# Performance work log

Measured on AMD Instinct MI355X. Metric: run time of the kernel, lower is better.

The kernel has to match this reference:

```python
import jax, jax.numpy as jnp
import numpy as np

N, E, G = 20000, 320000, 8
H, C = 4, 64
NODE_IN, EDGE_IN, HID = 18, 4, 64
NEG = 0.2    # GATv2 leaky_relu negative slope
EPS = 1e-5   # BatchNorm eps (eval mode: running_mean=0, running_var=1)


def setup_inputs() -> dict:
    key = jax.random.key(0)
    ks = iter(jax.random.split(key, 48))
    rn = lambda shape, s=0.05: jax.random.normal(next(ks), shape, dtype=jnp.float32) * s
    return {
        "x": jax.random.normal(next(ks), (N, NODE_IN), dtype=jnp.float32),
        "edge_attr": jax.random.uniform(next(ks), (E, EDGE_IN), dtype=jnp.float32),
        "enc_w1": rn((NODE_IN, HID)), "enc_b1": jnp.zeros((HID,), jnp.float32),
        "enc_w2": rn((HID, HID)), "enc_b2": jnp.zeros((HID,), jnp.float32),
        "g1_wl": rn((HID, H * C)), "g1_wr": rn((HID, H * C)), "g1_we": rn((EDGE_IN, H * C)),
        "g1_att": rn((H, C)), "g1_b": jnp.zeros((H * C,), jnp.float32),
        "bn1_g": jnp.ones((H * C,), jnp.float32), "bn1_b": jnp.zeros((H * C,), jnp.float32),
        "g2_wl": rn((H * C, H * C)), "g2_wr": rn((H * C, H * C)), "g2_we": rn((EDGE_IN, H * C)),
        "g2_att": rn((H, C)), "g2_b": jnp.zeros((C,), jnp.float32),
        "bn2_g": jnp.ones((C,), jnp.float32), "bn2_b": jnp.zeros((C,), jnp.float32),
        "sage_wl": rn((HID, HID)), "sage_bl": jnp.zeros((HID,), jnp.float32), "sage_wr": rn((HID, HID)),
        "bn3_g": jnp.ones((HID,), jnp.float32), "bn3_b": jnp.zeros((HID,), jnp.float32),
        "gh_w1": rn((2 * HID, HID)), "gh_b1": jnp.zeros((HID,), jnp.float32),
        "gh_w2": rn((HID, 32)), "gh_b2": jnp.zeros((32,), jnp.float32),
        "gh_w3": rn((32, 1)), "gh_b3": jnp.zeros((1,), jnp.float32),
        "eh_w1": rn((2 * HID + EDGE_IN, 32)), "eh_b1": jnp.zeros((32,), jnp.float32),
        "eh_w2": rn((32, 1)), "eh_b2": jnp.zeros((1,), jnp.float32),
        "edge_index": jax.random.randint(next(ks), (2, E), 0, N, dtype=jnp.int32),
        "batch": jnp.sort(jax.random.randint(next(ks), (N,), 0, G, dtype=jnp.int32)),
    }


def _segment_softmax(logits, seg, num):
    mx = jax.ops.segment_max(logits, seg, num_segments=num)
    ex = jnp.exp(logits - mx[seg])
    den = jax.ops.segment_sum(ex, seg, num_segments=num)
    return ex / den[seg]


def _gatv2(h, src, dst, ea, wl, wr, we, att, bias, concat):
    n = h.shape[0]
    xl = (h @ wl).reshape(n, H, C)   # messages come from x_l[src]
    xr = (h @ wr).reshape(n, H, C)
    ee = (ea @ we).reshape(-1, H, C)
    m = xl[src] + xr[dst] + ee                                    # [E', H, C]
    logit = jnp.einsum('ehc,hc->eh', jax.nn.leaky_relu(m, NEG), att)
    alpha = _segment_softmax(logit, dst, n)                       # [E', H]
    out = jax.ops.segment_sum(alpha[:, :, None] * xl[src], dst, num_segments=n)
    if concat:
        return out.reshape(n, H * C) + bias
    return out.mean(axis=1) + bias


def _bn_eval(h, g, b):
    # eval-mode BatchNorm with running_mean=0, running_var=1
    return h * (g / jnp.sqrt(1.0 + EPS)) + b


def reference(x, edge_attr, enc_w1, enc_b1, enc_w2, enc_b2,
              g1_wl, g1_wr, g1_we, g1_att, g1_b, bn1_g, bn1_b,
              g2_wl, g2_wr, g2_we, g2_att, g2_b, bn2_g, bn2_b,
              sage_wl, sage_bl, sage_wr, bn3_g, bn3_b,
              gh_w1, gh_b1, gh_w2, gh_b2, gh_w3, gh_b3,
              eh_w1, eh_b1, eh_w2, eh_b2, edge_index, batch):
    src, dst = edge_index[0], edge_index[1]
    # PyG add_self_loops with fill_value='mean': loop edge_attr = mean of incoming edge_attr
    ones = jnp.ones((E,), jnp.float32)
    cnt = jax.ops.segment_sum(ones, dst, num_segments=N)
    loop_attr = jax.ops.segment_sum(edge_attr, dst, num_segments=N) / jnp.clip(cnt, 1.0)[:, None]
    sl = jnp.arange(N, dtype=src.dtype)
    src_sl = jnp.concatenate([src, sl])
    dst_sl = jnp.concatenate([dst, sl])
    ea_sl = jnp.concatenate([edge_attr, loop_attr], axis=0)

    # ZoneEncoder (dropout inactive in eval)
    h = jax.nn.relu(x @ enc_w1 + enc_b1) @ enc_w2 + enc_b2
    h = _gatv2(h, src_sl, dst_sl, ea_sl, g1_wl, g1_wr, g1_we, g1_att, g1_b, True)
    h = jax.nn.elu(_bn_eval(h, bn1_g, bn1_b))
    h = _gatv2(h, src_sl, dst_sl, ea_sl, g2_wl, g2_wr, g2_we, g2_att, g2_b, False)
    h = jax.nn.elu(_bn_eval(h, bn2_g, bn2_b))
    # SAGEConv: lin_l(mean_{j->i} h_j) + lin_r(h_i), no self loops
    agg = jax.ops.segment_sum(h[src], dst, num_segments=N) / jnp.clip(cnt, 1.0)[:, None]
    h = agg @ sage_wl + sage_bl + h @ sage_wr
    h = jax.nn.relu(_bn_eval(h, bn3_g, bn3_b))
    # global mean + max pooling per graph
    cntg = jax.ops.segment_sum(jnp.ones((N,), jnp.float32), batch, num_segments=G)
    mean_p = jax.ops.segment_sum(h, batch, num_segments=G) / jnp.clip(cntg, 1.0)[:, None]
    max_p = jax.ops.segment_max(h, batch, num_segments=G)
    hp = jnp.concatenate([mean_p, max_p], axis=-1)                # [G, 128]
    z = jax.nn.relu(hp @ gh_w1 + gh_b1)
    z = jax.nn.relu(z @ gh_w2 + gh_b2)
    graph_score = jax.nn.sigmoid(z @ gh_w3 + gh_b3)               # [G, 1]
    ef = jnp.concatenate([h[src], h[dst], edge_attr], axis=-1)    # [E, 132]
    ez = jax.nn.relu(ef @ eh_w1 + eh_b1)
    edge_scores = jax.nn.sigmoid(ez @ eh_w2 + eh_b2)              # [E, 1]
    return (graph_score, edge_scores)
```

## Files before the change

kernel.cpp:

```cpp
#include <hip/hip_runtime.h>

#define NN 20000
#define NE 320000
#define EP (NE + NN)
#define NG 8
#define HC 256
#define NODE_IN 18
#define HID 64
#define NEG_SLOPE 0.2f
#define BN_EPS 1e-5f

#define OFF_XL    0u
#define OFF_XR    5120000u
#define OFF_H1    10240000u
#define OFF_WTL   12800000u
#define OFF_WTR   12832768u
#define OFF_H0    15360000u
#define OFF_H3    16640000u
#define OFF_ZERO  18000000u
#define OFF_CNT   18000000u
#define OFF_PSUM  18020000u
#define OFF_PMAX  18020512u
#define OFF_PCNT  18021024u
#define ZERO_FLOATS (18021040u - 18000000u)
#define OFF_EACSR 18021040u
#define OFF_RP    19381040u
#define OFF_SRC   19421041u
#define OFF_BSUM  19761056u

#define SCAN_ELEM 1024
#define SCAN_NB ((NN + SCAN_ELEM - 1) / SCAN_ELEM)

typedef __attribute__((ext_vector_type(8))) short bf16x8_t;
typedef __attribute__((ext_vector_type(4))) float f32x4_t;

__device__ __forceinline__ ushort f2bf(float f) {
  unsigned u = __float_as_uint(f);
  unsigned r = (u + 0x7fffu + ((u >> 16) & 1u)) >> 16;
  return (ushort)r;
}
__device__ __forceinline__ float bf2f(ushort b) {
  return __uint_as_float(((unsigned)b) << 16);
}

__global__ __launch_bounds__(256) void k_count(
    const int* __restrict__ ei, unsigned* __restrict__ cnt, int* __restrict__ rank) {
  int e = blockIdx.x * 256 + threadIdx.x;
  if (e >= NE) return;
  int d = ei[NE + e];
  rank[e] = (int)atomicAdd(&cnt[d], 1u);
}

__global__ __launch_bounds__(256) void k_cast_wt(
    const float* __restrict__ Wl, const float* __restrict__ Wr,
    ushort* __restrict__ WtL, ushort* __restrict__ WtR) {
  int b = blockIdx.x;
  const float* W = (b < 256) ? Wl : Wr;
  ushort* Wt = (b < 256) ? WtL : WtR;
  int k = b & 255;
  int n = threadIdx.x;
  Wt[n * 256 + k] = f2bf(W[k * 256 + n]);
}

#define ENC_NPW 4
__global__ __launch_bounds__(256) void k_encoder(
    const float* __restrict__ x, const float* __restrict__ w1, const float* __restrict__ b1,
    const float* __restrict__ w2, const float* __restrict__ b2, float* __restrict__ h0) {
  __shared__ float W1[NODE_IN * HID];
  __shared__ float W2[HID * HID];
  __shared__ float B1s[HID];
  __shared__ float B2s[HID];
  __shared__ float hid_s[4][HID];
  const int tid = threadIdx.x;
  for (int i = tid; i < NODE_IN * HID; i += 256) W1[i] = w1[i];
  for (int i = tid; i < HID * HID; i += 256) W2[i] = w2[i];
  if (tid < HID) { B1s[tid] = b1[tid]; B2s[tid] = b2[tid]; }
  __syncthreads();
  const int lane = tid & 63;
  const int w = tid >> 6;
  #pragma unroll
  for (int t = 0; t < ENC_NPW; t++) {
    const int n = blockIdx.x * (4 * ENC_NPW) + w * ENC_NPW + t;
    const float* xp = &x[(size_t)n * NODE_IN];
    float s = B1s[lane];
    #pragma unroll
    for (int i = 0; i < NODE_IN; i++) s += xp[i] * W1[i * HID + lane];
    hid_s[w][lane] = fmaxf(s, 0.f);
    float o = B2s[lane];
    #pragma unroll 8
    for (int k = 0; k < HID; k++) o += hid_s[w][k] * W2[k * HID + lane];
    h0[(size_t)n * HID + lane] = o;
  }
}

__global__ __launch_bounds__(256) void k_scan_blk(
    const unsigned* __restrict__ cnt, int* __restrict__ row_ptr, int* __restrict__ bsums) {
  __shared__ int wsum[4];
  const int tid = threadIdx.x, lane = tid & 63, w = tid >> 6;
  const int i0 = blockIdx.x * SCAN_ELEM + tid * 4;
  int v0 = (i0 + 0 < NN) ? ((int)cnt[i0 + 0] + 1) : 0;
  int v1 = (i0 + 1 < NN) ? ((int)cnt[i0 + 1] + 1) : 0;
  int v2 = (i0 + 2 < NN) ? ((int)cnt[i0 + 2] + 1) : 0;
  int v3 = (i0 + 3 < NN) ? ((int)cnt[i0 + 3] + 1) : 0;
  int tsum = v0 + v1 + v2 + v3;
  int incl = tsum;
  #pragma unroll
  for (int off = 1; off < 64; off <<= 1) {
    int t = __shfl_up(incl, off);
    if (lane >= off) incl += t;
  }
  if (lane == 63) wsum[w] = incl;
  __syncthreads();
  int p = incl - tsum;
  #pragma unroll
  for (int k = 0; k < 4; k++) if (k < w) p += wsum[k];
  if (i0 + 0 < NN) row_ptr[i0 + 0] = p;
  if (i0 + 1 < NN) row_ptr[i0 + 1] = p + v0;
  if (i0 + 2 < NN) row_ptr[i0 + 2] = p + v0 + v1;
  if (i0 + 3 < NN) row_ptr[i0 + 3] = p + v0 + v1 + v2;
  if (tid == 0) bsums[blockIdx.x] = wsum[0] + wsum[1] + wsum[2] + wsum[3];
}

__global__ __launch_bounds__(256) void k_scan_add(
    const int* __restrict__ bsums, int* __restrict__ row_ptr) {
  const int b = blockIdx.x, tid = threadIdx.x;
  int off = 0;
  for (int j = 0; j < b; j++) off += bsums[j];
  const int i0 = b * SCAN_ELEM + tid * 4;
  #pragma unroll
  for (int k = 0; k < 4; k++) {
    int i = i0 + k;
    if (i < NN) row_ptr[i] += off;
  }
  if (b == 0 && tid == 0) row_ptr[NN] = EP;
}

__global__ __launch_bounds__(256) void k_csr_scatter(
    const int* __restrict__ ei, const int* __restrict__ rank,
    const int* __restrict__ row_ptr, const float* __restrict__ ea,
    int* __restrict__ srcs, float* __restrict__ ea_csr) {
  int e = blockIdx.x * 256 + threadIdx.x;
  if (e >= NE) return;
  int s = ei[e], d = ei[NE + e];
  int p = row_ptr[d] + rank[e];
  srcs[p] = s;
  *(float4*)&ea_csr[(size_t)p * 4] = *(const float4*)&ea[(size_t)e * 4];
}

__global__ __launch_bounds__(256) void k_loop_row(
    const int* __restrict__ row_ptr, int* __restrict__ srcs, float* __restrict__ ea_csr) {
  int i = blockIdx.x * 256 + threadIdx.x;
  if (i >= NN) return;
  int start = row_ptr[i], last = row_ptr[i + 1] - 1;
  float sx = 0.f, sy = 0.f, sz = 0.f, sw = 0.f;
  for (int j = start; j < last; ++j) {
    float4 a = *(const float4*)&ea_csr[(size_t)j * 4];
    sx += a.x; sy += a.y; sz += a.z; sw += a.w;
  }
  float c = (float)(last - start);
  if (c < 1.f) c = 1.f;
  float rc = 1.f / c;
  float4 o = {sx * rc, sy * rc, sz * rc, sw * rc};
  *(float4*)&ea_csr[(size_t)last * 4] = o;
  srcs[last] = i | (int)0x80000000;
}

template <int K, int OBF>
__global__ __launch_bounds__(256) void k_gemm256(
    const float* __restrict__ A, const float* __restrict__ W, void* __restrict__ OUTv) {
  __shared__ float Wl[32 * 256];
  __shared__ float Al[32 * 36];
  const int tid = threadIdx.x;
  const int n0 = blockIdx.x * 32;
  const int tx = tid & 63, ty = tid >> 6;
  float acc[8][4];
  #pragma unroll
  for (int m = 0; m < 8; m++)
    #pragma unroll
    for (int c = 0; c < 4; c++) acc[m][c] = 0.f;

  for (int kt = 0; kt < K; kt += 32) {
    #pragma unroll
    for (int r = 0; r < 8; r++) {
      int i4 = tid + 256 * r;
      int row = i4 >> 6;
      int col4 = (i4 & 63) * 4;
      *(float4*)&Wl[row * 256 + col4] = *(const float4*)&W[(size_t)(kt + row) * 256 + col4];
    }
    {
      int m = tid >> 3, kk = (tid & 7) * 4;
      float4 av = *(const float4*)&A[(size_t)(n0 + m) * K + kt + kk];
      Al[(kk + 0) * 36 + m] = av.x;
      Al[(kk + 1) * 36 + m] = av.y;
      Al[(kk + 2) * 36 + m] = av.z;
      Al[(kk + 3) * 36 + m] = av.w;
    }
    __syncthreads();
    #pragma unroll 8
    for (int k = 0; k < 32; k++) {
      float4 b = *(float4*)&Wl[k * 256 + tx * 4];
      float4 a0v = *(float4*)&Al[k * 36 + ty * 8];
      float4 a1v = *(float4*)&Al[k * 36 + ty * 8 + 4];
      float am[8] = {a0v.x, a0v.y, a0v.z, a0v.w, a1v.x, a1v.y, a1v.z, a1v.w};
      #pragma unroll
      for (int m = 0; m < 8; m++) {
        acc[m][0] += am[m] * b.x;
        acc[m][1] += am[m] * b.y;
        acc[m][2] += am[m] * b.z;
        acc[m][3] += am[m] * b.w;
      }
    }
    __syncthreads();
  }
  if (OBF) {
    ushort* OUT = (ushort*)OUTv;
    #pragma unroll
    for (int m = 0; m < 8; m++) {
      ushort4 o = {f2bf(acc[m][0]), f2bf(acc[m][1]), f2bf(acc[m][2]), f2bf(acc[m][3])};
      *(ushort4*)&OUT[(size_t)(n0 + ty * 8 + m) * 256 + tx * 4] = o;
    }
  } else {
    float* OUT = (float*)OUTv;
    #pragma unroll
    for (int m = 0; m < 8; m++) {
      float4 o = {acc[m][0], acc[m][1], acc[m][2], acc[m][3]};
      *(float4*)&OUT[(size_t)(n0 + ty * 8 + m) * 256 + tx * 4] = o;
    }
  }
}

template <int OBF>
__global__ __launch_bounds__(256) void k_gemm_mfma(
    const ushort* __restrict__ A, const ushort* __restrict__ Wt, void* __restrict__ OUTv) {
  __shared__ ushort Asub[32][72];
  __shared__ ushort Wsub[256][72];
  const int tid = threadIdx.x;
  const int lane = tid & 63;
  const int w = tid >> 6;
  const int n0 = blockIdx.x * 32;
  const int lr = lane & 15;
  const int lk = (lane >> 4) * 8;

  f32x4_t acc[2][4];
  #pragma unroll
  for (int m = 0; m < 2; m++)
    #pragma unroll
    for (int n = 0; n < 4; n++) acc[m][n] = (f32x4_t){0.f, 0.f, 0.f, 0.f};

  for (int kt = 0; kt < 256; kt += 64) {
    {
      int r = tid >> 3, seg = (tid & 7) * 8;
      *(uint4*)&Asub[r][seg] = *(const uint4*)&A[(size_t)(n0 + r) * 256 + kt + seg];
    }
    #pragma unroll
    for (int rep = 0; rep < 8; rep++) {
      int idx = rep * 256 + tid;
      int r = idx >> 3, seg = (idx & 7) * 8;
      *(uint4*)&Wsub[r][seg] = *(const uint4*)&Wt[(size_t)r * 256 + kt + seg];
    }
    __syncthreads();
    #pragma unroll
    for (int kk = 0; kk < 2; kk++) {
      bf16x8_t af0 = *(bf16x8_t*)&Asub[lr][kk * 32 + lk];
      bf16x8_t af1 = *(bf16x8_t*)&Asub[16 + lr][kk * 32 + lk];
      #pragma unroll
      for (int n = 0; n < 4; n++) {
        bf16x8_t bfr = *(bf16x8_t*)&Wsub[w * 64 + n * 16 + lr][kk * 32 + lk];
        acc[0][n] = __builtin_amdgcn_mfma_f32_16x16x32_bf16(af0, bfr, acc[0][n], 0, 0, 0);
        acc[1][n] = __builtin_amdgcn_mfma_f32_16x16x32_bf16(af1, bfr, acc[1][n], 0, 0, 0);
      }
    }
    __syncthreads();
  }
  const int crow = (lane >> 4) * 4;
  #pragma unroll
  for (int m = 0; m < 2; m++) {
    #pragma unroll
    for (int n = 0; n < 4; n++) {
      int col = w * 64 + n * 16 + lr;
      #pragma unroll
      for (int r = 0; r < 4; r++) {
        int row = n0 + m * 16 + crow + r;
        if (OBF) ((ushort*)OUTv)[(size_t)row * 256 + col] = f2bf(acc[m][n][r]);
        else     ((float*)OUTv)[(size_t)row * 256 + col] = acc[m][n][r];
      }
    }
  }
}

#define GAT_EDGE(A_, U_, DN_, C0_, C1_, C2_, C3_)                                  \
  {                                                                                \
    float xx_ = bf2f((U_).x), xy_ = bf2f((U_).y), xz_ = bf2f((U_).z), xw_ = bf2f((U_).w); \
    float m0_ = xx_ + xrd.x + (A_).x * we0.x + (A_).y * we1.x + (A_).z * we2.x + (A_).w * we3.x; \
    float m1_ = xy_ + xrd.y + (A_).x * we0.y + (A_).y * we1.y + (A_).z * we2.y + (A_).w * we3.y; \
    float m2_ = xz_ + xrd.z + (A_).x * we0.z + (A_).y * we1.z + (A_).z * we2.z + (A_).w * we3.z; \
    float m3_ = xw_ + xrd.w + (A_).x * we0.w + (A_).y * we1.w + (A_).z * we2.w + (A_).w * we3.w; \
    m0_ = fmaxf(m0_, NEG_SLOPE * m0_);                                             \
    m1_ = fmaxf(m1_, NEG_SLOPE * m1_);                                             \
    m2_ = fmaxf(m2_, NEG_SLOPE * m2_);                                             \
    m3_ = fmaxf(m3_, NEG_SLOPE * m3_);                                             \
    float lg_ = m0_ * attv.x + m1_ * attv.y + m2_ * attv.z + m3_ * attv.w;         \
    lg_ += __shfl_xor(lg_, 1);                                                     \
    lg_ += __shfl_xor(lg_, 2);                                                     \
    lg_ += __shfl_xor(lg_, 4);                                                     \
    lg_ += __shfl_xor(lg_, 8);                                                     \
    float p_ = __expf(lg_);                                                        \
    DN_ += p_;                                                                     \
    C0_ = fmaf(p_, xx_, C0_);                                                      \
    C1_ = fmaf(p_, xy_, C1_);                                                      \
    C2_ = fmaf(p_, xz_, C2_);                                                      \
    C3_ = fmaf(p_, xw_, C3_);                                                      \
  }

template <int CONCAT>
__global__ __launch_bounds__(256) void k_gat_fused(
    const ushort* __restrict__ xl, const float* __restrict__ xr,
    const float* __restrict__ we, const float* __restrict__ att,
    const int* __restrict__ srcs, const float* __restrict__ ea_csr,
    const int* __restrict__ row_ptr,
    const float* __restrict__ bias, const float* __restrict__ bng,
    const float* __restrict__ bnb, void* __restrict__ outp) {
  const int lane = threadIdx.x & 63;
  const int w = threadIdx.x >> 6;
  const int i = blockIdx.x * 4 + w;
  const int c0 = lane * 4;

  const float4 attv = *(const float4*)&att[c0];
  const float4 we0 = *(const float4*)&we[0 * HC + c0];
  const float4 we1 = *(const float4*)&we[1 * HC + c0];
  const float4 we2 = *(const float4*)&we[2 * HC + c0];
  const float4 we3 = *(const float4*)&we[3 * HC + c0];
  const float4 xrd = *(const float4*)&xr[(size_t)i * HC + c0];

  const int start = row_ptr[i];
  const int deg = row_ptr[i + 1] - start;

  float dnA = 0.f, aA0 = 0.f, aA1 = 0.f, aA2 = 0.f, aA3 = 0.f;
  float dnB = 0.f, aB0 = 0.f, aB1 = 0.f, aB2 = 0.f, aB3 = 0.f;

  for (int base = 0; base < deg; base += 64) {
    int rem = deg - base;
    if (rem > 64) rem = 64;
    int sv = 0;
    if (lane < rem) sv = srcs[start + base + lane] & 0x7fffffff;
    int jj = 0;
    for (; jj + 2 <= rem; jj += 2) {
      int s0 = __shfl(sv, jj);
      int s1 = __shfl(sv, jj + 1);
      float4 a0 = *(const float4*)&ea_csr[(size_t)(start + base + jj) * 4];
      float4 a1 = *(const float4*)&ea_csr[(size_t)(start + base + jj + 1) * 4];
      ushort4 u0 = *(const ushort4*)&xl[(size_t)s0 * HC + c0];
      ushort4 u1 = *(const ushort4*)&xl[(size_t)s1 * HC + c0];
      GAT_EDGE(a0, u0, dnA, aA0, aA1, aA2, aA3);
      GAT_EDGE(a1, u1, dnB, aB0, aB1, aB2, aB3);
    }
    if (jj < rem) {
      int s0 = __shfl(sv, jj);
      float4 a0 = *(const float4*)&ea_csr[(size_t)(start + base + jj) * 4];
      ushort4 u0 = *(const ushort4*)&xl[(size_t)s0 * HC + c0];
      GAT_EDGE(a0, u0, dnA, aA0, aA1, aA2, aA3);
    }
  }

  float rinv = 1.f / (dnA + dnB);
  float acc0 = (aA0 + aB0) * rinv;
  float acc1 = (aA1 + aB1) * rinv;
  float acc2 = (aA2 + aB2) * rinv;
  float acc3 = (aA3 + aB3) * rinv;

  const float inv_sqrt = rsqrtf(1.f + BN_EPS);
  if (CONCAT) {
    float4 bi = *(const float4*)&bias[c0];
    float4 g = *(const float4*)&bng[c0];
    float4 bb = *(const float4*)&bnb[c0];
    float v0 = (acc0 + bi.x) * (g.x * inv_sqrt) + bb.x;
    float v1 = (acc1 + bi.y) * (g.y * inv_sqrt) + bb.y;
    float v2 = (acc2 + bi.z) * (g.z * inv_sqrt) + bb.z;
    float v3 = (acc3 + bi.w) * (g.w * inv_sqrt) + bb.w;
    v0 = (v0 > 0.f) ? v0 : (__expf(v0) - 1.f);
    v1 = (v1 > 0.f) ? v1 : (__expf(v1) - 1.f);
    v2 = (v2 > 0.f) ? v2 : (__expf(v2) - 1.f);
    v3 = (v3 > 0.f) ? v3 : (__expf(v3) - 1.f);
    ushort* op = (ushort*)outp;
    ushort4 o = {f2bf(v0), f2bf(v1), f2bf(v2), f2bf(v3)};
    *(ushort4*)&op[(size_t)i * HC + c0] = o;
  } else {
    acc0 += __shfl_xor(acc0, 16); acc0 += __shfl_xor(acc0, 32);
    acc1 += __shfl_xor(acc1, 16); acc1 += __shfl_xor(acc1, 32);
    acc2 += __shfl_xor(acc2, 16); acc2 += __shfl_xor(acc2, 32);
    acc3 += __shfl_xor(acc3, 16); acc3 += __shfl_xor(acc3, 32);
    if (lane < 16) {
      int cc = lane * 4;
      float4 bi = *(const float4*)&bias[cc];
      float4 g = *(const float4*)&bng[cc];
      float4 bb = *(const float4*)&bnb[cc];
      float v0 = (0.25f * acc0 + bi.x) * (g.x * inv_sqrt) + bb.x;
      float v1 = (0.25f * acc1 + bi.y) * (g.y * inv_sqrt) + bb.y;
      float v2 = (0.25f * acc2 + bi.z) * (g.z * inv_sqrt) + bb.z;
      float v3 = (0.25f * acc3 + bi.w) * (g.w * inv_sqrt) + bb.w;
      v0 = (v0 > 0.f) ? v0 : (__expf(v0) - 1.f);
      v1 = (v1 > 0.f) ? v1 : (__expf(v1) - 1.f);
      v2 = (v2 > 0.f) ? v2 : (__expf(v2) - 1.f);
      v3 = (v3 > 0.f) ? v3 : (__expf(v3) - 1.f);
      float* op = (float*)outp;
      float4 o = {v0, v1, v2, v3};
      *(float4*)&op[(size_t)i * 64 + cc] = o;
    }
  }
}

__global__ __launch_bounds__(256) void k_sage(
    const float* __restrict__ h2, const int* __restrict__ row_ptr,
    const int* __restrict__ srcs, const unsigned* __restrict__ cnt,
    const float* __restrict__ wl, const float* __restrict__ bl,
    const float* __restrict__ wr, const float* __restrict__ bng,
    const float* __restrict__ bnb, float* __restrict__ h3) {
  __shared__ float agg_s[4][64];
  __shared__ float h2_s[4][64];
  int lane = threadIdx.x & 63;
  int w = threadIdx.x >> 6;
  int i = blockIdx.x * 4 + w;
  int start = row_ptr[i];
  int nreal = row_ptr[i + 1] - 1 - start;
  float a0 = 0.f, a1 = 0.f, a2 = 0.f, a3 = 0.f;
  for (int base = 0; base < nreal; base += 64) {
    int rem = nreal - base;
    if (rem > 64) rem = 64;
    int sv = 0;
    if (lane < rem) sv = srcs[start + base + lane];
    int jj = 0;
    for (; jj + 4 <= rem; jj += 4) {
      int s0 = __shfl(sv, jj);
      int s1 = __shfl(sv, jj + 1);
      int s2 = __shfl(sv, jj + 2);
      int s3 = __shfl(sv, jj + 3);
      a0 += h2[(size_t)s0 * 64 + lane];
      a1 += h2[(size_t)s1 * 64 + lane];
      a2 += h2[(size_t)s2 * 64 + lane];
      a3 += h2[(size_t)s3 * 64 + lane];
    }
    for (; jj < rem; ++jj) {
      int s0 = __shfl(sv, jj);
      a0 += h2[(size_t)s0 * 64 + lane];
    }
  }
  float a = (a0 + a1) + (a2 + a3);
  float c = (float)cnt[i];
  if (c < 1.f) c = 1.f;
  agg_s[w][lane] = a / c;
  h2_s[w][lane] = h2[(size_t)i * 64 + lane];
  __syncthreads();
  float s = bl[lane];
  #pragma unroll 4
  for (int k = 0; k < 64; k++)
    s += agg_s[w][k] * wl[k * 64 + lane] + h2_s[w][k] * wr[k * 64 + lane];
  s = s * (bng[lane] * rsqrtf(1.f + BN_EPS)) + bnb[lane];
  s = fmaxf(s, 0.f);
  h3[(size_t)i * 64 + lane] = s;
}

__global__ __launch_bounds__(256) void k_pool(
    const float* __restrict__ h3, const int* __restrict__ batch,
    float* __restrict__ psum, float* __restrict__ pmax, float* __restrict__ pcnt) {
  int j = threadIdx.x & 63, grp = threadIdx.x >> 6;
  int nbase = blockIdx.x * 256 + grp * 64;
  float s = 0.f, m = 0.f, cn = 0.f;
  int cur = -1;
  for (int t = 0; t < 64; t++) {
    int n = nbase + t;
    if (n >= NN) break;
    int g = batch[n];
    if (g != cur) {
      if (cur >= 0) {
        atomicAdd(&psum[cur * 64 + j], s);
        atomicMax((int*)&pmax[cur * 64 + j], __float_as_int(m));
        if (j == 0) atomicAdd(&pcnt[cur], cn);
      }
      cur = g; s = 0.f; m = 0.f; cn = 0.f;
    }
    float v = h3[(size_t)n * 64 + j];
    s += v; m = fmaxf(m, v); cn += 1.f;
  }
  if (cur >= 0) {
    atomicAdd(&psum[cur * 64 + j], s);
    atomicMax((int*)&pmax[cur * 64 + j], __float_as_int(m));
    if (j == 0) atomicAdd(&pcnt[cur], cn);
  }
}

__global__ void k_graph_head(
    const float* __restrict__ psum, const float* __restrict__ pmax,
    const float* __restrict__ pcnt,
    const float* __restrict__ w1, const float* __restrict__ b1,
    const float* __restrict__ w2, const float* __restrict__ b2,
    const float* __restrict__ w3, const float* __restrict__ b3,
    float* __restrict__ out) {
  __shared__ float hp[128];
  __shared__ float z1[64];
  __shared__ float z2[32];
  int g = blockIdx.x, j = threadIdx.x;
  float c = pcnt[g];
  if (c < 1.f) c = 1.f;
  hp[j] = psum[g * 64 + j] / c;
  hp[64 + j] = pmax[g * 64 + j];
  __syncthreads();
  float s = b1[j];
  #pragma unroll 8
  for (int k = 0; k < 128; k++) s += hp[k] * w1[k * 64 + j];
  z1[j] = fmaxf(s, 0.f);
  __syncthreads();
  if (j < 32) {
    float s2 = b2[j];
    #pragma unroll 8
    for (int k = 0; k < 64; k++) s2 += z1[k] * w2[k * 32 + j];
    z2[j] = fmaxf(s2, 0.f);
  }
  __syncthreads();
  if (j == 0) {
    float s3 = b3[0];
    #pragma unroll
    for (int k = 0; k < 32; k++) s3 += z2[k] * w3[k];
    out[g] = 1.f / (1.f + expf(-s3));
  }
}

__global__ __launch_bounds__(256) void k_edge_head(
    const float* __restrict__ h3, const int* __restrict__ ei,
    const float* __restrict__ ea,
    const float* __restrict__ w1, const float* __restrict__ b1,
    const float* __restrict__ w2, const float* __restrict__ b2,
    float* __restrict__ out) {
  int e = blockIdx.x * 256 + threadIdx.x;
  if (e >= NE) return;
  int s = ei[e], d = ei[NE + e];
  float acc[32];
  #pragma unroll
  for (int j = 0; j < 32; j++) acc[j] = b1[j];
  const float4* hs = (const float4*)&h3[(size_t)s * 64];
  const float4* hd = (const float4*)&h3[(size_t)d * 64];
  for (int k4 = 0; k4 < 16; k4++) {
    float4 v = hs[k4];
    const float* w = &w1[k4 * 4 * 32];
    #pragma unroll
    for (int j = 0; j < 32; j++) acc[j] += v.x * w[j];
    #pragma unroll
    for (int j = 0; j < 32; j++) acc[j] += v.y * w[32 + j];
    #pragma unroll
    for (int j = 0; j < 32; j++) acc[j] += v.z * w[64 + j];
    #pragma unroll
    for (int j = 0; j < 32; j++) acc[j] += v.w * w[96 + j];
  }
  for (int k4 = 0; k4 < 16; k4++) {
    float4 v = hd[k4];
    const float* w = &w1[(64 + k4 * 4) * 32];
    #pragma unroll
    for (int j = 0; j < 32; j++) acc[j] += v.x * w[j];
    #pragma unroll
    for (int j = 0; j < 32; j++) acc[j] += v.y * w[32 + j];
    #pragma unroll
    for (int j = 0; j < 32; j++) acc[j] += v.z * w[64 + j];
    #pragma unroll
    for (int j = 0; j < 32; j++) acc[j] += v.w * w[96 + j];
  }
  {
    float4 v = *(const float4*)&ea[(size_t)e * 4];
    const float* w = &w1[128 * 32];
    #pragma unroll
    for (int j = 0; j < 32; j++) acc[j] += v.x * w[j];
    #pragma unroll
    for (int j = 0; j < 32; j++) acc[j] += v.y * w[32 + j];
    #pragma unroll
    for (int j = 0; j < 32; j++) acc[j] += v.z * w[64 + j];
    #pragma unroll
    for (int j = 0; j < 32; j++) acc[j] += v.w * w[96 + j];
  }
  float s2 = b2[0];
  #pragma unroll
  for (int j = 0; j < 32; j++) s2 += fmaxf(acc[j], 0.f) * w2[j];
  out[e] = 1.f / (1.f + expf(-s2));
}

extern "C" void kernel_launch(void* const* d_in, const int* in_sizes, int n_in,
                              void* d_out, int out_size, void* d_ws, size_t ws_size,
                              hipStream_t stream) {
  const float* x         = (const float*)d_in[0];
  const float* edge_attr = (const float*)d_in[1];
  const float* enc_w1 = (const float*)d_in[2];
  const float* enc_b1 = (const float*)d_in[3];
  const float* enc_w2 = (const float*)d_in[4];
  const float* enc_b2 = (const float*)d_in[5];
  const float* g1_wl = (const float*)d_in[6];
  const float* g1_wr = (const float*)d_in[7];
  const float* g1_we = (const float*)d_in[8];
  const float* g1_att = (const float*)d_in[9];
  const float* g1_b = (const float*)d_in[10];
  const float* bn1_g = (const float*)d_in[11];
  const float* bn1_b = (const float*)d_in[12];
  const float* g2_wl = (const float*)d_in[13];
  const float* g2_wr = (const float*)d_in[14];
  const float* g2_we = (const float*)d_in[15];
  const float* g2_att = (const float*)d_in[16];
  const float* g2_b = (const float*)d_in[17];
  const float* bn2_g = (const float*)d_in[18];
  const float* bn2_b = (const float*)d_in[19];
  const float* sage_wl = (const float*)d_in[20];
  const float* sage_bl = (const float*)d_in[21];
  const float* sage_wr = (const float*)d_in[22];
  const float* bn3_g = (const float*)d_in[23];
  const float* bn3_b = (const float*)d_in[24];
  const float* gh_w1 = (const float*)d_in[25];
  const float* gh_b1 = (const float*)d_in[26];
  const float* gh_w2 = (const float*)d_in[27];
  const float* gh_b2 = (const float*)d_in[28];
  const float* gh_w3 = (const float*)d_in[29];
  const float* gh_b3 = (const float*)d_in[30];
  const float* eh_w1 = (const float*)d_in[31];
  const float* eh_b1 = (const float*)d_in[32];
  const float* eh_w2 = (const float*)d_in[33];
  const float* eh_b2 = (const float*)d_in[34];
  const int* ei    = (const int*)d_in[35];
  const int* batch = (const int*)d_in[36];
  float* out = (float*)d_out;

  float* ws = (float*)d_ws;
  ushort* xlbf = (ushort*)(ws + OFF_XL);
  float* xr = ws + OFF_XR;
  ushort* h1bf = (ushort*)(ws + OFF_H1);
  ushort* wtl = (ushort*)(ws + OFF_WTL);
  ushort* wtr = (ushort*)(ws + OFF_WTR);
  float* h0 = ws + OFF_H0;
  float* h3 = ws + OFF_H3;
  unsigned* cnt = (unsigned*)(ws + OFF_CNT);
  float* psum = ws + OFF_PSUM;
  float* pmax = ws + OFF_PMAX;
  float* pcnt = ws + OFF_PCNT;
  float* ea_csr = ws + OFF_EACSR;
  int* row_ptr = (int*)(ws + OFF_RP);
  int* srcs = (int*)(ws + OFF_SRC);
  int* bsums = (int*)(ws + OFF_BSUM);
  int* rank = (int*)(ws + OFF_XL);

  hipMemsetAsync(ws + OFF_ZERO, 0, ZERO_FLOATS * sizeof(float), stream);

  k_count<<<NE / 256, 256, 0, stream>>>(ei, cnt, rank);
  k_cast_wt<<<512, 256, 0, stream>>>(g2_wl, g2_wr, wtl, wtr);
  k_encoder<<<NN / (4 * ENC_NPW), 256, 0, stream>>>(x, enc_w1, enc_b1, enc_w2, enc_b2, h0);
  k_scan_blk<<<SCAN_NB, 256, 0, stream>>>(cnt, row_ptr, bsums);
  k_scan_add<<<SCAN_NB, 256, 0, stream>>>(bsums, row_ptr);
  k_csr_scatter<<<NE / 256, 256, 0, stream>>>(ei, rank, row_ptr, edge_attr, srcs, ea_csr);
  k_loop_row<<<(NN + 255) / 256, 256, 0, stream>>>(row_ptr, srcs, ea_csr);

  k_gemm256<64, 1><<<NN / 32, 256, 0, stream>>>(h0, g1_wl, (void*)xlbf);
  k_gemm256<64, 0><<<NN / 32, 256, 0, stream>>>(h0, g1_wr, (void*)xr);
  k_gat_fused<1><<<NN / 4, 256, 0, stream>>>(xlbf, xr, g1_we, g1_att, srcs, ea_csr,
                                             row_ptr, g1_b, bn1_g, bn1_b, (void*)h1bf);

  k_gemm_mfma<1><<<NN / 32, 256, 0, stream>>>(h1bf, wtl, (void*)xlbf);
  k_gemm_mfma<0><<<NN / 32, 256, 0, stream>>>(h1bf, wtr, (void*)xr);
  k_gat_fused<0><<<NN / 4, 256, 0, stream>>>(xlbf, xr, g2_we, g2_att, srcs, ea_csr,
                                             row_ptr, g2_b, bn2_g, bn2_b, (void*)h0);

  k_sage<<<NN / 4, 256, 0, stream>>>(h0, row_ptr, srcs, cnt, sage_wl, sage_bl, sage_wr, bn3_g, bn3_b, h3);

  k_pool<<<(NN + 255) / 256, 256, 0, stream>>>(h3, batch, psum, pmax, pcnt);
  k_graph_head<<<NG, 64, 0, stream>>>(psum, pmax, pcnt, gh_w1, gh_b1, gh_w2, gh_b2, gh_w3, gh_b3, out);
  k_edge_head<<<NE / 256, 256, 0, stream>>>(h3, ei, edge_attr, eh_w1, eh_b1, eh_w2, eh_b2, out + NG);
}
```

Before: 360.3 us.

## Compute edge head MLP with bf16 MFMA on gathered node features

Rewrites the per-edge MLP head so each block gathers 64 edges' source/destination features (from a new bf16 copy of h3 written by the SAGE kernel) plus edge attributes into LDS. It then computes the 132x32 layer with 16x16x32 bf16 MFMA instructions instead of per-thread scalar FMAs over 32 accumulators. A small kernel pre-transposes and zero-pads the head weights to bf16. This removes a heavy scalar-FMA and register-bound workload and halves gather bytes, at the cost of bf16 precision in the edge scores and an extra bf16 store in SAGE.

```diff
diff --git a/kernel.cpp b/kernel.cpp
--- a/kernel.cpp
+++ b/kernel.cpp
@@ -15,6 +15,8 @@
 #define OFF_H1    10240000u
 #define OFF_WTL   12800000u
 #define OFF_WTR   12832768u
+#define OFF_H3B   12865536u
+#define OFF_WT1   13185536u
 #define OFF_H0    15360000u
 #define OFF_H3    16640000u
 #define OFF_ZERO  18000000u
@@ -60,6 +62,13 @@
   int k = b & 255;
   int n = threadIdx.x;
   Wt[n * 256 + k] = f2bf(W[k * 256 + n]);
+}
+
+__global__ __launch_bounds__(256) void k_cast_eh(
+    const float* __restrict__ w1, ushort* __restrict__ wt1) {
+  int idx = blockIdx.x * 256 + threadIdx.x;
+  int n = idx / 192, k = idx - n * 192;
+  wt1[idx] = (k < 132) ? f2bf(w1[k * 32 + n]) : (ushort)0;
 }
 
 #define ENC_NPW 4
@@ -414,7 +423,8 @@
     const int* __restrict__ srcs, const unsigned* __restrict__ cnt,
     const float* __restrict__ wl, const float* __restrict__ bl,
     const float* __restrict__ wr, const float* __restrict__ bng,
-    const float* __restrict__ bnb, float* __restrict__ h3) {
+    const float* __restrict__ bnb, float* __restrict__ h3,
+    ushort* __restrict__ h3b) {
   __shared__ float agg_s[4][64];
   __shared__ float h2_s[4][64];
   int lane = threadIdx.x & 63;
@@ -457,6 +467,7 @@
   s = s * (bng[lane] * rsqrtf(1.f + BN_EPS)) + bnb[lane];
   s = fmaxf(s, 0.f);
   h3[(size_t)i * 64 + lane] = s;
+  h3b[(size_t)i * 64 + lane] = f2bf(s);
 }
 
 __global__ __launch_bounds__(256) void k_pool(
@@ -525,59 +536,71 @@
 }
 
 __global__ __launch_bounds__(256) void k_edge_head(
-    const float* __restrict__ h3, const int* __restrict__ ei,
-    const float* __restrict__ ea,
-    const float* __restrict__ w1, const float* __restrict__ b1,
-    const float* __restrict__ w2, const float* __restrict__ b2,
-    float* __restrict__ out) {
-  int e = blockIdx.x * 256 + threadIdx.x;
-  if (e >= NE) return;
-  int s = ei[e], d = ei[NE + e];
-  float acc[32];
-  #pragma unroll
-  for (int j = 0; j < 32; j++) acc[j] = b1[j];
-  const float4* hs = (const float4*)&h3[(size_t)s * 64];
-  const float4* hd = (const float4*)&h3[(size_t)d * 64];
-  for (int k4 = 0; k4 < 16; k4++) {
-    float4 v = hs[k4];
-    const float* w = &w1[k4 * 4 * 32];
-    #pragma unroll
-    for (int j = 0; j < 32; j++) acc[j] += v.x * w[j];
-    #pragma unroll
-    for (int j = 0; j < 32; j++) acc[j] += v.y * w[32 + j];
-    #pragma unroll
-    for (int j = 0; j < 32; j++) acc[j] += v.z * w[64 + j];
-    #pragma unroll
-    for (int j = 0; j < 32; j++) acc[j] += v.w * w[96 + j];
-  }
-  for (int k4 = 0; k4 < 16; k4++) {
-    float4 v = hd[k4];
-    const float* w = &w1[(64 + k4 * 4) * 32];
-    #pragma unroll
-    for (int j = 0; j < 32; j++) acc[j] += v.x * w[j];
-    #pragma unroll
-    for (int j = 0; j < 32; j++) acc[j] += v.y * w[32 + j];
-    #pragma unroll
-    for (int j = 0; j < 32; j++) acc[j] += v.z * w[64 + j];
-    #pragma unroll
-    for (int j = 0; j < 32; j++) acc[j] += v.w * w[96 + j];
-  }
-  {
-    float4 v = *(const float4*)&ea[(size_t)e * 4];
-    const float* w = &w1[128 * 32];
-    #pragma unroll
-    for (int j = 0; j < 32; j++) acc[j] += v.x * w[j];
-    #pragma unroll
-    for (int j = 0; j < 32; j++) acc[j] += v.y * w[32 + j];
-    #pragma unroll
-    for (int j = 0; j < 32; j++) acc[j] += v.z * w[64 + j];
-    #pragma unroll
-    for (int j = 0; j < 32; j++) acc[j] += v.w * w[96 + j];
-  }
-  float s2 = b2[0];
-  #pragma unroll
-  for (int j = 0; j < 32; j++) s2 += fmaxf(acc[j], 0.f) * w2[j];
-  out[e] = 1.f / (1.f + expf(-s2));
+    const ushort* __restrict__ h3b, const int* __restrict__ ei,
+    const float* __restrict__ ea, const ushort* __restrict__ wt1,
+    const float* __restrict__ b1, const float* __restrict__ w2,
+    const float* __restrict__ b2, float* __restrict__ out) {
+  __shared__ ushort Asub[64][192];
+  __shared__ ushort Wsub[32][192];
+  const int tid = threadIdx.x;
+  const int e0 = blockIdx.x * 64;
+  for (int idx = tid; idx < 768; idx += 256)
+    *(uint4*)&(&Wsub[0][0])[idx * 8] = *(const uint4*)&wt1[idx * 8];
+  for (int idx = tid; idx < 768; idx += 256) {
+    int r = idx / 12, g = idx - r * 12;
+    int e = e0 + r;
+    ushort tmp[16];
+    if (g < 8) {
+      int node = (g < 4) ? ei[e] : ei[NE + e];
+      int gc = (g & 3) * 16;
+      *(uint4*)&tmp[0] = *(const uint4*)&h3b[(size_t)node * 64 + gc];
+      *(uint4*)&tmp[8] = *(const uint4*)&h3b[(size_t)node * 64 + gc + 8];
+    } else if (g == 8) {
+      float4 a = *(const float4*)&ea[(size_t)e * 4];
+      tmp[0] = f2bf(a.x); tmp[1] = f2bf(a.y); tmp[2] = f2bf(a.z); tmp[3] = f2bf(a.w);
+      #pragma unroll
+      for (int j = 4; j < 16; j++) tmp[j] = 0;
+    } else {
+      #pragma unroll
+      for (int j = 0; j < 16; j++) tmp[j] = 0;
+    }
+    *(uint4*)&Asub[r][g * 16] = *(uint4*)&tmp[0];
+    *(uint4*)&Asub[r][g * 16 + 8] = *(uint4*)&tmp[8];
+  }
+  __syncthreads();
+  const int lane = tid & 63, wid = tid >> 6;
+  const int lr = lane & 15, lk = (lane >> 4) * 8;
+  f32x4_t acc0 = (f32x4_t){0.f, 0.f, 0.f, 0.f};
+  f32x4_t acc1 = (f32x4_t){0.f, 0.f, 0.f, 0.f};
+  #pragma unroll
+  for (int ks = 0; ks < 6; ks++) {
+    bf16x8_t af = *(bf16x8_t*)&Asub[wid * 16 + lr][ks * 32 + lk];
+    bf16x8_t bw0 = *(bf16x8_t*)&Wsub[lr][ks * 32 + lk];
+    bf16x8_t bw1 = *(bf16x8_t*)&Wsub[16 + lr][ks * 32 + lk];
+    acc0 = __builtin_amdgcn_mfma_f32_16x16x32_bf16(af, bw0, acc0, 0, 0, 0);
+    acc1 = __builtin_amdgcn_mfma_f32_16x16x32_bf16(af, bw1, acc1, 0, 0, 0);
+  }
+  float b1c0 = b1[lr], b1c1 = b1[16 + lr];
+  float w2c0 = w2[lr], w2c1 = w2[16 + lr];
+  float part[4];
+  #pragma unroll
+  for (int r = 0; r < 4; r++) {
+    float v0 = fmaxf(acc0[r] + b1c0, 0.f) * w2c0;
+    float v1 = fmaxf(acc1[r] + b1c1, 0.f) * w2c1;
+    float p = v0 + v1;
+    p += __shfl_xor(p, 1);
+    p += __shfl_xor(p, 2);
+    p += __shfl_xor(p, 4);
+    p += __shfl_xor(p, 8);
+    part[r] = p;
+  }
+  if (lr == 0) {
+    const float bb2 = b2[0];
+    int ebase = e0 + wid * 16 + (lane >> 4) * 4;
+    #pragma unroll
+    for (int r = 0; r < 4; r++)
+      out[ebase + r] = 1.f / (1.f + __expf(-(part[r] + bb2)));
+  }
 }
 
 extern "C" void kernel_launch(void* const* d_in, const int* in_sizes, int n_in,
@@ -628,6 +651,8 @@
   ushort* h1bf = (ushort*)(ws + OFF_H1);
   ushort* wtl = (ushort*)(ws + OFF_WTL);
   ushort* wtr = (ushort*)(ws + OFF_WTR);
+  ushort* h3b = (ushort*)(ws + OFF_H3B);
+  ushort* wt1e = (ushort*)(ws + OFF_WT1);
   float* h0 = ws + OFF_H0;
   float* h3 = ws + OFF_H3;
   unsigned* cnt = (unsigned*)(ws + OFF_CNT);
@@ -644,6 +669,7 @@
 
   k_count<<<NE / 256, 256, 0, stream>>>(ei, cnt, rank);
   k_cast_wt<<<512, 256, 0, stream>>>(g2_wl, g2_wr, wtl, wtr);
+  k_cast_eh<<<24, 256, 0, stream>>>(eh_w1, wt1e);
   k_encoder<<<NN / (4 * ENC_NPW), 256, 0, stream>>>(x, enc_w1, enc_b1, enc_w2, enc_b2, h0);
   k_scan_blk<<<SCAN_NB, 256, 0, stream>>>(cnt, row_ptr, bsums);
   k_scan_add<<<SCAN_NB, 256, 0, stream>>>(bsums, row_ptr);
@@ -660,9 +686,10 @@
   k_gat_fused<0><<<NN / 4, 256, 0, stream>>>(xlbf, xr, g2_we, g2_att, srcs, ea_csr,
                                              row_ptr, g2_b, bn2_g, bn2_b, (void*)h0);
 
-  k_sage<<<NN / 4, 256, 0, stream>>>(h0, row_ptr, srcs, cnt, sage_wl, sage_bl, sage_wr, bn3_g, bn3_b, h3);
+  k_sage<<<NN / 4, 256, 0, stream>>>(h0, row_ptr, srcs, cnt, sage_wl, sage_bl, sage_wr,
+                                     bn3_g, bn3_b, h3, h3b);
 
   k_pool<<<(NN + 255) / 256, 256, 0, stream>>>(h3, batch, psum, pmax, pcnt);
   k_graph_head<<<NG, 64, 0, stream>>>(psum, pmax, pcnt, gh_w1, gh_b1, gh_w2, gh_b2, gh_w3, gh_b3, out);
-  k_edge_head<<<NE / 256, 256, 0, stream>>>(h3, ei, edge_attr, eh_w1, eh_b1, eh_w2, eh_b2, out + NG);
-}
+  k_edge_head<<<NE / 64, 256, 0, stream>>>(h3b, ei, edge_attr, wt1e, eh_b1, eh_w2, eh_b2, out + NG);
+}
```

Measured after the change: 346.8 us. 1.04x faster.
